# Optimization experiments

Hardware: AMD Instinct MI355X
Metric: run time of the kernel (lower is better)

## Reference

```python
import jax, jax.numpy as jnp
import numpy as np

N = 100_000      # nodes
E = 3_200_000    # edges (avg degree 32)
F_IN = 172       # raw node features
HID = 32         # hid_channels
ENC = 8          # encoding_dim
H, C = 2, 16     # heads, per-head channels (TransformerConv 32 -> 2x16)
OUT = 2          # classes
INV_SQRT_C = 1.0 / np.sqrt(C).astype(np.float32)


def setup_inputs() -> dict:
    key = jax.random.key(0)
    ks = jax.random.split(key, 40)
    p = lambda k, shape: (jax.random.normal(k, shape, dtype=jnp.float32) * 0.05)
    return {
        # data tensors
        "x": jax.random.normal(ks[0], (N, F_IN), dtype=jnp.float32),
        "edge_index": jax.random.randint(ks[1], (2, E), 0, N),
        "node_time": jax.random.uniform(ks[2], (N,), dtype=jnp.float32),
        "edge_time": jax.random.uniform(ks[3], (E, 1), dtype=jnp.float32),
        "node_interval": jax.random.uniform(ks[4], (N, 1), dtype=jnp.float32),
        "node_degree": jax.random.uniform(ks[5], (N, 1), dtype=jnp.float32),
        # TimeEncode(32): cos(Linear(1, 32))
        "Wt": p(ks[6], (1, HID)), "bt": p(ks[7], (HID,)),
        # DegreeEncoder / TemporalFrequencyEncoder: Linear(1, 8)
        "Wd": p(ks[8], (1, ENC)), "bd": p(ks[9], (ENC,)),
        "Wtf": p(ks[10], (1, ENC)), "btf": p(ks[11], (ENC,)),
        # w_enc: Linear(8, 8); w_x: Linear(32, 8)
        "Wenc": p(ks[12], (ENC, ENC)), "benc": p(ks[13], (ENC,)),
        "Wx": p(ks[14], (HID, ENC)), "bx": p(ks[15], (ENC,)),
        # lin: Linear(in_channels, 32)
        "Wlin": p(ks[16], (F_IN, HID)), "blin": p(ks[17], (HID,)),
        # lin_combine: Linear(40, 32)
        "Wcomb": p(ks[18], (HID + ENC, HID)), "bcomb": p(ks[19], (HID,)),
        # TransformerConv projections (32 -> heads*16 = 32)
        "Wq": p(ks[20], (HID, H * C)), "bq": p(ks[21], (H * C,)),
        "Wk": p(ks[22], (HID, H * C)), "bk": p(ks[23], (H * C,)),
        "Wv": p(ks[24], (HID, H * C)), "bv": p(ks[25], (H * C,)),
        "We": p(ks[26], (HID, H * C)), "be": p(ks[27], (H * C,)),
        "Wskip": p(ks[28], (HID, H * C)), "bskip": p(ks[29], (H * C,)),
        # out: Linear(32, out_channels)
        "Wout": p(ks[30], (HID, OUT)), "bout": p(ks[31], (OUT,)),
    }


def _segment_softmax(alpha, seg, num_segments):
    # alpha: [E, H], seg: [E] destination indices
    m = jax.ops.segment_max(alpha, seg, num_segments=num_segments)
    a = jnp.exp(alpha - m[seg])
    s = jax.ops.segment_sum(a, seg, num_segments=num_segments)
    return a / (s[seg] + 1e-16)


def reference(x, edge_index, node_time, edge_time, node_interval, node_degree,
              Wt, bt, Wd, bd, Wtf, btf, Wenc, benc, Wx, bx, Wlin, blin,
              Wcomb, bcomb, Wq, bq, Wk, bk, Wv, bv, We, be, Wskip, bskip,
              Wout, bout):
    src, dst = edge_index[0], edge_index[1]
    n = x.shape[0]

    # ---- time encoding of relative edge time: cos(Linear(rel_t)) ----
    rel_t = node_time[src][:, None] - edge_time               # [E, 1]
    rel_t_enc = jnp.cos(rel_t @ Wt + bt)                      # [E, 32]

    # ---- node encoders + attention-gated combine ----
    h1 = x @ Wlin + blin                                      # [N, 32]
    tf_enc = node_interval @ Wtf + btf                        # [N, 8]
    deg_enc = node_degree @ Wd + bd                           # [N, 8]
    encodings = jnp.stack((tf_enc, deg_enc), axis=1)          # [N, 2, 8]
    enc_proj = jnp.tanh(encodings @ Wenc + benc)              # [N, 2, 8]
    x_proj = jnp.tanh(h1 @ Wx + bx)                           # [N, 8]
    score = jnp.einsum('nke,ne->nk', enc_proj, x_proj)        # [N, 2]
    score = jax.nn.softmax(score, axis=1)
    context = jnp.einsum('nke,nk->ne', encodings, score)      # [N, 8]
    h1 = jnp.concatenate((h1, context), axis=1) @ Wcomb + bcomb  # [N, 32]

    # ---- TransformerConv (heads=2, out=16, concat) with edge features ----
    q = (h1 @ Wq + bq).reshape(n, H, C)
    k = (h1 @ Wk + bk).reshape(n, H, C)
    v = (h1 @ Wv + bv).reshape(n, H, C)
    e = (rel_t_enc @ We + be).reshape(-1, H, C)               # [E, H, C]

    k_e = k[src] + e                                          # [E, H, C]
    alpha = jnp.einsum('ehc,ehc->eh', q[dst], k_e) * INV_SQRT_C
    alpha = _segment_softmax(alpha, dst, n)                   # [E, H]
    msg = (v[src] + e) * alpha[..., None]                     # [E, H, C]
    agg = jax.ops.segment_sum(msg, dst, num_segments=n)       # [N, H, C]
    h2 = agg.reshape(n, H * C) + (h1 @ Wskip + bskip)         # root_weight skip

    out = h2 @ Wout + bout                                    # [N, 2]
    return jax.nn.log_softmax(out, axis=1)
```

## Files before the change

kernel.cpp:

```cpp
#include <hip/hip_runtime.h>
#include <hip/hip_bf16.h>
#include <cstdint>


#define FIN 172
#define INV_SQRT_C 0.25f

typedef _Float16 f16x8 __attribute__((ext_vector_type(8)));
typedef float f32x4 __attribute__((ext_vector_type(4)));

__device__ __forceinline__ uint32_t cvt_pk_bf16(float lo, float hi) {
    uint32_t r;
    asm("v_cvt_pk_bf16_f32 %0, %1, %2" : "=v"(r) : "v"(lo), "v"(hi));
    return r;
}
__device__ __forceinline__ float bflo(uint32_t u) {
    union { uint32_t i; float f; } x; x.i = u << 16; return x.f;
}
__device__ __forceinline__ float bfhi(uint32_t u) {
    union { uint32_t i; float f; } x; x.i = u & 0xFFFF0000u; return x.f;
}
__device__ __forceinline__ void pk_atomic_add_bf16(void* addr, uint32_t data) {
    asm volatile("global_atomic_pk_add_bf16 %0, %1, off"
                 :: "v"((uint64_t)(uintptr_t)addr), "v"(data) : "memory");
}

__global__ __launch_bounds__(256) void k1_lin(
    const float* __restrict__ x, const float* __restrict__ Wlin,
    const float* __restrict__ blin, float* __restrict__ h1pre, int n)
{
    const int lane = threadIdx.x & 63;
    const int g = lane >> 4, m = lane & 15;

    f16x8 Bf[6][2];
    #pragma unroll
    for (int s = 0; s < 6; ++s) {
        #pragma unroll
        for (int i = 0; i < 8; ++i) {
            const int k = s * 32 + g * 8 + i;
            Bf[s][0][i] = (_Float16)((k < FIN) ? Wlin[k * 32 + m] : 0.f);
            Bf[s][1][i] = (_Float16)((k < FIN) ? Wlin[k * 32 + 16 + m] : 0.f);
        }
    }
    const float b0 = blin[m], b1 = blin[16 + m];

    const int wid = blockIdx.x * 4 + (threadIdx.x >> 6);
    const int nW  = gridDim.x * 4;
    const int nChunks = (n + 15) / 16;

    for (int c = wid; c < nChunks; c += nW) {
        const int row = c * 16 + m;
        const bool rv = row < n;
        const float* xr = x + (size_t)row * FIN;

        f32x4 acc0 = {0.f, 0.f, 0.f, 0.f};
        f32x4 acc1 = {0.f, 0.f, 0.f, 0.f};
        #pragma unroll
        for (int s = 0; s < 6; ++s) {
            f16x8 A;
            #pragma unroll
            for (int i = 0; i < 8; ++i) {
                const int k = s * 32 + g * 8 + i;
                A[i] = (_Float16)((rv && k < FIN) ? xr[k] : 0.f);
            }
            acc0 = __builtin_amdgcn_mfma_f32_16x16x32_f16(A, Bf[s][0], acc0, 0, 0, 0);
            acc1 = __builtin_amdgcn_mfma_f32_16x16x32_f16(A, Bf[s][1], acc1, 0, 0, 0);
        }
        #pragma unroll
        for (int r = 0; r < 4; ++r) {
            const int node = c * 16 + 4 * g + r;
            if (node < n) {
                h1pre[(size_t)node * 32 + m]      = acc0[r] + b0;
                h1pre[(size_t)node * 32 + 16 + m] = acc1[r] + b1;
            }
        }
    }
}

template <int K, int O>
__device__ __forceinline__ void matvecKO(const float* __restrict__ v,
                                         const float* __restrict__ W,
                                         const float* __restrict__ B,
                                         float* __restrict__ out)
{
    #pragma unroll
    for (int o4 = 0; o4 < O / 4; ++o4) {
        float a0 = B[o4 * 4 + 0], a1 = B[o4 * 4 + 1];
        float a2 = B[o4 * 4 + 2], a3 = B[o4 * 4 + 3];
        #pragma unroll
        for (int k = 0; k < K; ++k) {
            float4 wv = *reinterpret_cast<const float4*>(&W[k * O + o4 * 4]);
            float hv = v[k];
            a0 = fmaf(hv, wv.x, a0);
            a1 = fmaf(hv, wv.y, a1);
            a2 = fmaf(hv, wv.z, a2);
            a3 = fmaf(hv, wv.w, a3);
        }
        out[o4 * 4 + 0] = a0; out[o4 * 4 + 1] = a1;
        out[o4 * 4 + 2] = a2; out[o4 * 4 + 3] = a3;
    }
}

__global__ __launch_bounds__(256) void k2_enc(
    const float* __restrict__ h1pre,
    const float* __restrict__ node_interval, const float* __restrict__ node_degree,
    const float* __restrict__ Wtf, const float* __restrict__ btf,
    const float* __restrict__ Wd,  const float* __restrict__ bd,
    const float* __restrict__ Wenc, const float* __restrict__ benc,
    const float* __restrict__ Wx,  const float* __restrict__ bx,
    const float* __restrict__ Wcomb, const float* __restrict__ bcomb,
    const float* __restrict__ Wq,  const float* __restrict__ bq,
    const float* __restrict__ Wk,  const float* __restrict__ bk,
    const float* __restrict__ Wv,  const float* __restrict__ bv,
    const float* __restrict__ Wskip, const float* __restrict__ bskip,
    uint32_t* __restrict__ q32, uint32_t* __restrict__ kv32,
    float* __restrict__ skipb, int n)
{
    __shared__ __align__(16) float sWenc[64], sWx[256];
    __shared__ float sWtf[8], sbtf[8], sWd[8], sbd[8], sbenc[8], sbx[8];
    __shared__ __align__(16) _Float16 v40s[256][72];
    __shared__ __align__(16) _Float16 h1s[256][40];

    const int t = threadIdx.x;
    if (t < 8) {
        sWtf[t] = Wtf[t]; sbtf[t] = btf[t];
        sWd[t]  = Wd[t];  sbd[t]  = bd[t];
        sbenc[t] = benc[t]; sbx[t] = bx[t];
    }
    if (t < 64) sWenc[t] = Wenc[t];
    if (t < 256) sWx[t] = Wx[t];

    const int nid = blockIdx.x * 256 + t;
    const bool active = nid < n;

    __syncthreads();

    if (active) {
        float h1p[32];
        const float2* hp = reinterpret_cast<const float2*>(h1pre + (size_t)nid * 32);
        #pragma unroll
        for (int i = 0; i < 16; ++i) {
            float2 v2 = hp[i];
            h1p[2 * i] = v2.x; h1p[2 * i + 1] = v2.y;
        }
        const float ti = node_interval[nid], dg = node_degree[nid];
        float tf[8], de[8];
        #pragma unroll
        for (int j = 0; j < 8; ++j) {
            tf[j] = fmaf(ti, sWtf[j], sbtf[j]);
            de[j] = fmaf(dg, sWd[j], sbd[j]);
        }
        float xp[8];
        matvecKO<32, 8>(h1p, sWx, sbx, xp);
        #pragma unroll
        for (int o = 0; o < 8; ++o) xp[o] = tanhf(xp[o]);

        float ep0[8], ep1[8];
        matvecKO<8, 8>(tf, sWenc, sbenc, ep0);
        matvecKO<8, 8>(de, sWenc, sbenc, ep1);
        float sc0 = 0.f, sc1 = 0.f;
        #pragma unroll
        for (int o = 0; o < 8; ++o) {
            sc0 = fmaf(tanhf(ep0[o]), xp[o], sc0);
            sc1 = fmaf(tanhf(ep1[o]), xp[o], sc1);
        }
        const float mm = fmaxf(sc0, sc1);
        const float e0 = __expf(sc0 - mm), e1 = __expf(sc1 - mm);
        const float inv = 1.f / (e0 + e1);
        const float s0 = e0 * inv, s1 = e1 * inv;

        #pragma unroll
        for (int i = 0; i < 32; ++i) v40s[t][i] = (_Float16)h1p[i];
        #pragma unroll
        for (int j = 0; j < 8; ++j)
            v40s[t][32 + j] = (_Float16)fmaf(s0, tf[j], s1 * de[j]);
    } else {
        #pragma unroll
        for (int i = 0; i < 40; ++i) v40s[t][i] = (_Float16)0.f;
    }
    #pragma unroll
    for (int i = 40; i < 64; ++i) v40s[t][i] = (_Float16)0.f;

    __syncthreads();

    const int lane = t & 63;
    const int g = lane >> 4, m = lane & 15;
    const int wv = t >> 6;
    const int node0 = blockIdx.x * 256;

    f16x8 Bc0[2], Bc1[2];
    #pragma unroll
    for (int s = 0; s < 2; ++s)
        #pragma unroll
        for (int i = 0; i < 8; ++i) {
            const int k = s * 32 + g * 8 + i;
            Bc0[s][i] = (_Float16)((k < 40) ? Wcomb[k * 32 + m] : 0.f);
            Bc1[s][i] = (_Float16)((k < 40) ? Wcomb[k * 32 + 16 + m] : 0.f);
        }
    const float bc0 = bcomb[m], bc1 = bcomb[16 + m];

    for (int c = wv; c < 16; c += 4) {
        f32x4 a0 = {0.f, 0.f, 0.f, 0.f};
        f32x4 a1 = {0.f, 0.f, 0.f, 0.f};
        #pragma unroll
        for (int s = 0; s < 2; ++s) {
            const f16x8 A = *reinterpret_cast<const f16x8*>(&v40s[c * 16 + m][s * 32 + g * 8]);
            a0 = __builtin_amdgcn_mfma_f32_16x16x32_f16(A, Bc0[s], a0, 0, 0, 0);
            a1 = __builtin_amdgcn_mfma_f32_16x16x32_f16(A, Bc1[s], a1, 0, 0, 0);
        }
        #pragma unroll
        for (int r = 0; r < 4; ++r) {
            const int nb = c * 16 + 4 * g + r;
            h1s[nb][m]      = (_Float16)(a0[r] + bc0);
            h1s[nb][16 + m] = (_Float16)(a1[r] + bc1);
        }
    }
    __syncthreads();

    f16x8 Bq0, Bq1, Bk0, Bk1, Bv0, Bv1, Bs0, Bs1;
    #pragma unroll
    for (int i = 0; i < 8; ++i) {
        const int k = g * 8 + i;
        Bq0[i] = (_Float16)Wq[k * 32 + m];     Bq1[i] = (_Float16)Wq[k * 32 + 16 + m];
        Bk0[i] = (_Float16)Wk[k * 32 + m];     Bk1[i] = (_Float16)Wk[k * 32 + 16 + m];
        Bv0[i] = (_Float16)Wv[k * 32 + m];     Bv1[i] = (_Float16)Wv[k * 32 + 16 + m];
        Bs0[i] = (_Float16)Wskip[k * 32 + m];  Bs1[i] = (_Float16)Wskip[k * 32 + 16 + m];
    }
    const float bq0 = bq[m], bq1 = bq[16 + m];
    const float bk0 = bk[m], bk1 = bk[16 + m];
    const float bv0 = bv[m], bv1 = bv[16 + m];
    const float bs0 = bskip[m], bs1 = bskip[16 + m];

    for (int c = wv; c < 16; c += 4) {
        const f16x8 A = *reinterpret_cast<const f16x8*>(&h1s[c * 16 + m][g * 8]);

        f32x4 aq0 = {0.f,0.f,0.f,0.f}, aq1 = {0.f,0.f,0.f,0.f};
        f32x4 ak0 = {0.f,0.f,0.f,0.f}, ak1 = {0.f,0.f,0.f,0.f};
        f32x4 av0 = {0.f,0.f,0.f,0.f}, av1 = {0.f,0.f,0.f,0.f};
        f32x4 as0 = {0.f,0.f,0.f,0.f}, as1 = {0.f,0.f,0.f,0.f};
        aq0 = __builtin_amdgcn_mfma_f32_16x16x32_f16(A, Bq0, aq0, 0, 0, 0);
        aq1 = __builtin_amdgcn_mfma_f32_16x16x32_f16(A, Bq1, aq1, 0, 0, 0);
        ak0 = __builtin_amdgcn_mfma_f32_16x16x32_f16(A, Bk0, ak0, 0, 0, 0);
        ak1 = __builtin_amdgcn_mfma_f32_16x16x32_f16(A, Bk1, ak1, 0, 0, 0);
        av0 = __builtin_amdgcn_mfma_f32_16x16x32_f16(A, Bv0, av0, 0, 0, 0);
        av1 = __builtin_amdgcn_mfma_f32_16x16x32_f16(A, Bv1, av1, 0, 0, 0);
        as0 = __builtin_amdgcn_mfma_f32_16x16x32_f16(A, Bs0, as0, 0, 0, 0);
        as1 = __builtin_amdgcn_mfma_f32_16x16x32_f16(A, Bs1, as1, 0, 0, 0);

        #pragma unroll
        for (int r = 0; r < 4; ++r) {
            const int node = node0 + c * 16 + 4 * g + r;
            if (node < n) {
                q32[(size_t)node * 16 + m] =
                    cvt_pk_bf16(aq0[r] + bq0, aq1[r] + bq1);
                uint2 kvd;
                kvd.x = cvt_pk_bf16(ak0[r] + bk0, ak1[r] + bk1);
                kvd.y = cvt_pk_bf16(av0[r] + bv0, av1[r] + bv1);
                *reinterpret_cast<uint2*>(kv32 + (size_t)node * 32 + 2 * m) = kvd;
                skipb[(size_t)node * 32 + m]      = as0[r] + bs0;
                skipb[(size_t)node * 32 + 16 + m] = as1[r] + bs1;
            }
        }
    }
}

__global__ __launch_bounds__(256) void k3_edge(
    const int* __restrict__ ei, const float* __restrict__ node_time,
    const float* __restrict__ edge_time,
    const uint32_t* __restrict__ qp, const uint32_t* __restrict__ kvp,
    const float* __restrict__ Wt, const float* __restrict__ bt,
    const float* __restrict__ We, const float* __restrict__ be,
    unsigned short* __restrict__ agg, unsigned short* __restrict__ den,
    int numE, int nTiles)
{
    const int lane = threadIdx.x & 63;
    const int g = lane >> 4;
    const int m = lane & 15;

    float wtr[8], btr[8];
    f16x8 B0, B1;
    #pragma unroll
    for (int i = 0; i < 8; ++i) {
        const int k = g * 8 + i;
        wtr[i] = Wt[k];
        btr[i] = bt[k];
        B0[i] = (_Float16)We[k * 32 + m];
        B1[i] = (_Float16)We[k * 32 + 16 + m];
    }
    const float be0 = be[m], be1 = be[16 + m];

    const int wid = blockIdx.x * (blockDim.x >> 6) + (threadIdx.x >> 6);
    const int nW  = gridDim.x * (blockDim.x >> 6);

    int tile = wid;
    if (tile >= nTiles) return;

    int srcm = 0, dstm = 0;
    float et = 0.f;
    {
        const int eA = tile * 16 + m;
        if (eA < numE) {
            srcm = ei[eA];
            dstm = ei[numE + eA];
            et   = edge_time[eA];
        }
    }

    while (true) {
        const float nt = node_time[srcm];
        int srcr[4], dstr[4];
        uint32_t qw[4];
        uint2 kvw[4];
        #pragma unroll
        for (int r = 0; r < 4; ++r) {
            const int j = g * 4 + r;
            srcr[r] = __shfl(srcm, j);
            dstr[r] = __shfl(dstm, j);
            qw[r]  = qp[(size_t)dstr[r] * 16 + m];
            kvw[r] = *reinterpret_cast<const uint2*>(
                         kvp + (size_t)srcr[r] * 32 + 2 * m);
        }

        const int ntile = tile + nW;
        int nsrc = 0, ndst = 0;
        float net = 0.f;
        if (ntile < nTiles) {
            const int eA = ntile * 16 + m;
            if (eA < numE) {
                nsrc = ei[eA];
                ndst = ei[numE + eA];
                net  = edge_time[eA];
            }
        }

        const float rel = nt - et;
        f16x8 A;
        #pragma unroll
        for (int i = 0; i < 8; ++i)
            A[i] = (_Float16)__cosf(fmaf(rel, wtr[i], btr[i]));

        f32x4 acc0 = {0.f, 0.f, 0.f, 0.f};
        f32x4 acc1 = {0.f, 0.f, 0.f, 0.f};
        acc0 = __builtin_amdgcn_mfma_f32_16x16x32_f16(A, B0, acc0, 0, 0, 0);
        acc1 = __builtin_amdgcn_mfma_f32_16x16x32_f16(A, B1, acc1, 0, 0, 0);

        const int e0 = tile * 16;
        #pragma unroll
        for (int r = 0; r < 4; ++r) {
            if (e0 + g * 4 + r < numE) {
                const float ef0 = acc0[r] + be0;
                const float ef1 = acc1[r] + be1;

                const uint32_t uq = qw[r];
                const uint32_t uk = kvw[r].x, uv = kvw[r].y;
                const float q0 = bflo(uq), q1 = bfhi(uq);
                const float k0 = bflo(uk), k1 = bfhi(uk);
                const float v0 = bflo(uv), v1 = bfhi(uv);

                float p0 = q0 * (k0 + ef0);
                float p1 = q1 * (k1 + ef1);
                #pragma unroll
                for (int s = 1; s < 16; s <<= 1) {
                    p0 += __shfl_xor(p0, s);
                    p1 += __shfl_xor(p1, s);
                }
                const float w0 = __expf(p0 * INV_SQRT_C);
                const float w1 = __expf(p1 * INV_SQRT_C);

                const float t0 = w0 * (v0 + ef0);
                const float t1 = w1 * (v1 + ef1);
                const float x0 = __shfl_xor(t0, 1);
                const float x1 = __shfl_xor(t1, 1);
                const uint32_t data = (m & 1) ? cvt_pk_bf16(x1, t1)
                                              : cvt_pk_bf16(t0, x0);
                const int choff = (m & 1) ? (15 + m) : m;
                pk_atomic_add_bf16(agg + (size_t)dstr[r] * 32 + choff, data);

                if (m == 0)
                    pk_atomic_add_bf16(den + (size_t)dstr[r] * 2,
                                       cvt_pk_bf16(w0, w1));
            }
        }

        if (ntile >= nTiles) break;
        tile = ntile; srcm = nsrc; dstm = ndst; et = net;
    }
}

__global__ __launch_bounds__(256) void k4_out(
    const unsigned short* __restrict__ agg, const unsigned short* __restrict__ den,
    const float* __restrict__ skipb,
    const float* __restrict__ Wout, const float* __restrict__ bout,
    float* __restrict__ out, int n)
{
    __shared__ float sW[64];
    __shared__ float sb[2];
    const int t = threadIdx.x;
    if (t < 64) sW[t] = Wout[t];
    if (t < 2) sb[t] = bout[t];
    __syncthreads();

    const int nid = blockIdx.x * 256 + t;
    if (nid >= n) return;

    const uint32_t ud = reinterpret_cast<const uint32_t*>(den)[nid];
    const float inv0 = 1.f / (bflo(ud) + 1e-16f);
    const float inv1 = 1.f / (bfhi(ud) + 1e-16f);
    const uint32_t* ag = reinterpret_cast<const uint32_t*>(agg) + (size_t)nid * 16;
    const float*    sk = skipb + (size_t)nid * 32;

    float o0 = sb[0], o1 = sb[1];
    #pragma unroll
    for (int p = 0; p < 16; ++p) {
        const uint32_t u = ag[p];
        const float iv = (p < 8) ? inv0 : inv1;
        const float hLo = fmaf(bflo(u), iv, sk[2 * p]);
        const float hHi = fmaf(bfhi(u), iv, sk[2 * p + 1]);
        o0 = fmaf(hLo, sW[(2 * p) * 2],     o0);
        o1 = fmaf(hLo, sW[(2 * p) * 2 + 1], o1);
        o0 = fmaf(hHi, sW[(2 * p + 1) * 2],     o0);
        o1 = fmaf(hHi, sW[(2 * p + 1) * 2 + 1], o1);
    }
    const float mm = fmaxf(o0, o1);
    const float lse = mm + __logf(__expf(o0 - mm) + __expf(o1 - mm));
    out[(size_t)nid * 2 + 0] = o0 - lse;
    out[(size_t)nid * 2 + 1] = o1 - lse;
}

extern "C" void kernel_launch(void* const* d_in, const int* in_sizes, int n_in,
                              void* d_out, int out_size, void* d_ws, size_t ws_size,
                              hipStream_t stream)
{
    const float* x             = (const float*)d_in[0];
    const int*   ei            = (const int*)  d_in[1];
    const float* node_time     = (const float*)d_in[2];
    const float* edge_time     = (const float*)d_in[3];
    const float* node_interval = (const float*)d_in[4];
    const float* node_degree   = (const float*)d_in[5];
    const float* Wt    = (const float*)d_in[6];  const float* bt    = (const float*)d_in[7];
    const float* Wd    = (const float*)d_in[8];  const float* bd    = (const float*)d_in[9];
    const float* Wtf   = (const float*)d_in[10]; const float* btf   = (const float*)d_in[11];
    const float* Wenc  = (const float*)d_in[12]; const float* benc  = (const float*)d_in[13];
    const float* Wx    = (const float*)d_in[14]; const float* bx    = (const float*)d_in[15];
    const float* Wlin  = (const float*)d_in[16]; const float* blin  = (const float*)d_in[17];
    const float* Wcomb = (const float*)d_in[18]; const float* bcomb = (const float*)d_in[19];
    const float* Wq    = (const float*)d_in[20]; const float* bq    = (const float*)d_in[21];
    const float* Wk    = (const float*)d_in[22]; const float* bk    = (const float*)d_in[23];
    const float* Wv    = (const float*)d_in[24]; const float* bv    = (const float*)d_in[25];
    const float* We    = (const float*)d_in[26]; const float* be    = (const float*)d_in[27];
    const float* Wskip = (const float*)d_in[28]; const float* bskip = (const float*)d_in[29];
    const float* Wout  = (const float*)d_in[30]; const float* bout  = (const float*)d_in[31];

    const int n    = in_sizes[2];
    const int numE = in_sizes[3];

    char* base = (char*)d_ws;
    uint32_t* q32  = (uint32_t*)base; base += (size_t)n * 16 * 4;
    uint32_t* kv32 = (uint32_t*)base; base += (size_t)n * 32 * 4;
    float* skipb = (float*)base; base += (size_t)n * 32 * 4;
    float* h1pre = (float*)base; base += (size_t)n * 32 * 4;
    unsigned short* agg = (unsigned short*)base; base += (size_t)n * 32 * 2;
    unsigned short* den = (unsigned short*)base; base += (size_t)n * 2 * 2;

    hipMemsetAsync(agg, 0, (size_t)n * (32 * 2 + 2 * 2), stream);

    k1_lin<<<512, 256, 0, stream>>>(x, Wlin, blin, h1pre, n);

    k2_enc<<<(n + 255) / 256, 256, 0, stream>>>(
        h1pre, node_interval, node_degree,
        Wtf, btf, Wd, bd, Wenc, benc, Wx, bx, Wcomb, bcomb,
        Wq, bq, Wk, bk, Wv, bv, Wskip, bskip,
        q32, kv32, skipb, n);

    const int nTiles = (numE + 15) / 16;
    k3_edge<<<4096, 256, 0, stream>>>(
        ei, node_time, edge_time, q32, kv32,
        Wt, bt, We, be, agg, den, numE, nTiles);

    k4_out<<<(n + 255) / 256, 256, 0, stream>>>(
        agg, den, skipb, Wout, bout, (float*)d_out, n);
}
```

Baseline: 423.0 us.

## Project edge messages and skip through Wout before aggregation to shrink atomics

Uses linearity of the final Wout projection: each edge message is reduced per head to two output logits through a 16-lane shuffle reduction. Each edge then issues three small packed-bf16 atomics (head0 logits, head1 logits, softmax denominators) in place of a 32-channel atomic row plus a denominator atomic. The skip path is likewise projected to two floats in k2, which cuts skip buffer traffic. The cost is extra shuffle reductions per edge, and summing projected values in bf16 may change rounding error.

```diff
diff --git a/kernel.cpp b/kernel.cpp
--- a/kernel.cpp
+++ b/kernel.cpp
@@ -113,8 +113,9 @@
     const float* __restrict__ Wk,  const float* __restrict__ bk,
     const float* __restrict__ Wv,  const float* __restrict__ bv,
     const float* __restrict__ Wskip, const float* __restrict__ bskip,
+    const float* __restrict__ Wout,
     uint32_t* __restrict__ q32, uint32_t* __restrict__ kv32,
-    float* __restrict__ skipb, int n)
+    float2* __restrict__ skip2, int n)
 {
     __shared__ __align__(16) float sWenc[64], sWx[256];
     __shared__ float sWtf[8], sbtf[8], sWd[8], sbd[8], sbenc[8], sbx[8];
@@ -230,6 +231,8 @@
     const float bk0 = bk[m], bk1 = bk[16 + m];
     const float bv0 = bv[m], bv1 = bv[16 + m];
     const float bs0 = bskip[m], bs1 = bskip[16 + m];
+    const float wo00 = Wout[m * 2],        wo01 = Wout[m * 2 + 1];
+    const float wo10 = Wout[(16 + m) * 2], wo11 = Wout[(16 + m) * 2 + 1];
 
     for (int c = wv; c < 16; c += 4) {
         const f16x8 A = *reinterpret_cast<const f16x8*>(&h1s[c * 16 + m][g * 8]);
@@ -250,6 +253,14 @@
         #pragma unroll
         for (int r = 0; r < 4; ++r) {
             const int node = node0 + c * 16 + 4 * g + r;
+            const float sv0 = as0[r] + bs0, sv1 = as1[r] + bs1;
+            float u0 = fmaf(sv0, wo00, sv1 * wo10);
+            float u1 = fmaf(sv0, wo01, sv1 * wo11);
+            #pragma unroll
+            for (int s = 1; s < 16; s <<= 1) {
+                u0 += __shfl_xor(u0, s);
+                u1 += __shfl_xor(u1, s);
+            }
             if (node < n) {
                 q32[(size_t)node * 16 + m] =
                     cvt_pk_bf16(aq0[r] + bq0, aq1[r] + bq1);
@@ -257,8 +268,7 @@
                 kvd.x = cvt_pk_bf16(ak0[r] + bk0, ak1[r] + bk1);
                 kvd.y = cvt_pk_bf16(av0[r] + bv0, av1[r] + bv1);
                 *reinterpret_cast<uint2*>(kv32 + (size_t)node * 32 + 2 * m) = kvd;
-                skipb[(size_t)node * 32 + m]      = as0[r] + bs0;
-                skipb[(size_t)node * 32 + 16 + m] = as1[r] + bs1;
+                if (m == 0) skip2[node] = make_float2(u0, u1);
             }
         }
     }
@@ -270,8 +280,8 @@
     const uint32_t* __restrict__ qp, const uint32_t* __restrict__ kvp,
     const float* __restrict__ Wt, const float* __restrict__ bt,
     const float* __restrict__ We, const float* __restrict__ be,
-    unsigned short* __restrict__ agg, unsigned short* __restrict__ den,
-    int numE, int nTiles)
+    const float* __restrict__ Wout,
+    unsigned short* __restrict__ acc, int numE, int nTiles)
 {
     const int lane = threadIdx.x & 63;
     const int g = lane >> 4;
@@ -288,6 +298,8 @@
         B1[i] = (_Float16)We[k * 32 + 16 + m];
     }
     const float be0 = be[m], be1 = be[16 + m];
+    const float wo00 = Wout[m * 2],        wo01 = Wout[m * 2 + 1];
+    const float wo10 = Wout[(16 + m) * 2], wo11 = Wout[(16 + m) * 2 + 1];
 
     const int wid = blockIdx.x * (blockDim.x >> 6) + (threadIdx.x >> 6);
     const int nW  = gridDim.x * (blockDim.x >> 6);
@@ -369,16 +381,18 @@
 
                 const float t0 = w0 * (v0 + ef0);
                 const float t1 = w1 * (v1 + ef1);
-                const float x0 = __shfl_xor(t0, 1);
-                const float x1 = __shfl_xor(t1, 1);
-                const uint32_t data = (m & 1) ? cvt_pk_bf16(x1, t1)
-                                              : cvt_pk_bf16(t0, x0);
-                const int choff = (m & 1) ? (15 + m) : m;
-                pk_atomic_add_bf16(agg + (size_t)dstr[r] * 32 + choff, data);
-
-                if (m == 0)
-                    pk_atomic_add_bf16(den + (size_t)dstr[r] * 2,
-                                       cvt_pk_bf16(w0, w1));
+                float u00 = t0 * wo00, u01 = t0 * wo01;
+                float u10 = t1 * wo10, u11 = t1 * wo11;
+                #pragma unroll
+                for (int s = 1; s < 16; s <<= 1) {
+                    u00 += __shfl_xor(u00, s); u01 += __shfl_xor(u01, s);
+                    u10 += __shfl_xor(u10, s); u11 += __shfl_xor(u11, s);
+                }
+
+                unsigned short* row = acc + (size_t)dstr[r] * 32;
+                if (m == 0) pk_atomic_add_bf16(row,     cvt_pk_bf16(u00, u01));
+                if (m == 1) pk_atomic_add_bf16(row + 2, cvt_pk_bf16(u10, u11));
+                if (m == 2) pk_atomic_add_bf16(row + 4, cvt_pk_bf16(w0,  w1));
             }
         }
 
@@ -388,39 +402,20 @@
 }
 
 __global__ __launch_bounds__(256) void k4_out(
-    const unsigned short* __restrict__ agg, const unsigned short* __restrict__ den,
-    const float* __restrict__ skipb,
-    const float* __restrict__ Wout, const float* __restrict__ bout,
-    float* __restrict__ out, int n)
-{
-    __shared__ float sW[64];
-    __shared__ float sb[2];
-    const int t = threadIdx.x;
-    if (t < 64) sW[t] = Wout[t];
-    if (t < 2) sb[t] = bout[t];
-    __syncthreads();
-
-    const int nid = blockIdx.x * 256 + t;
+    const unsigned short* __restrict__ acc, const float2* __restrict__ skip2,
+    const float* __restrict__ bout, float* __restrict__ out, int n)
+{
+    const int nid = blockIdx.x * 256 + threadIdx.x;
     if (nid >= n) return;
 
-    const uint32_t ud = reinterpret_cast<const uint32_t*>(den)[nid];
-    const float inv0 = 1.f / (bflo(ud) + 1e-16f);
-    const float inv1 = 1.f / (bfhi(ud) + 1e-16f);
-    const uint32_t* ag = reinterpret_cast<const uint32_t*>(agg) + (size_t)nid * 16;
-    const float*    sk = skipb + (size_t)nid * 32;
-
-    float o0 = sb[0], o1 = sb[1];
-    #pragma unroll
-    for (int p = 0; p < 16; ++p) {
-        const uint32_t u = ag[p];
-        const float iv = (p < 8) ? inv0 : inv1;
-        const float hLo = fmaf(bflo(u), iv, sk[2 * p]);
-        const float hHi = fmaf(bfhi(u), iv, sk[2 * p + 1]);
-        o0 = fmaf(hLo, sW[(2 * p) * 2],     o0);
-        o1 = fmaf(hLo, sW[(2 * p) * 2 + 1], o1);
-        o0 = fmaf(hHi, sW[(2 * p + 1) * 2],     o0);
-        o1 = fmaf(hHi, sW[(2 * p + 1) * 2 + 1], o1);
-    }
+    const uint4 u = *reinterpret_cast<const uint4*>(acc + (size_t)nid * 32);
+    const float inv0 = 1.f / (bflo(u.z) + 1e-16f);
+    const float inv1 = 1.f / (bfhi(u.z) + 1e-16f);
+    const float2 sk = skip2[nid];
+
+    const float o0 = bflo(u.x) * inv0 + bflo(u.y) * inv1 + sk.x + bout[0];
+    const float o1 = bfhi(u.x) * inv0 + bfhi(u.y) * inv1 + sk.y + bout[1];
+
     const float mm = fmaxf(o0, o1);
     const float lse = mm + __logf(__expf(o0 - mm) + __expf(o1 - mm));
     out[(size_t)nid * 2 + 0] = o0 - lse;
@@ -457,26 +452,25 @@
     char* base = (char*)d_ws;
     uint32_t* q32  = (uint32_t*)base; base += (size_t)n * 16 * 4;
     uint32_t* kv32 = (uint32_t*)base; base += (size_t)n * 32 * 4;
-    float* skipb = (float*)base; base += (size_t)n * 32 * 4;
     float* h1pre = (float*)base; base += (size_t)n * 32 * 4;
-    unsigned short* agg = (unsigned short*)base; base += (size_t)n * 32 * 2;
-    unsigned short* den = (unsigned short*)base; base += (size_t)n * 2 * 2;
-
-    hipMemsetAsync(agg, 0, (size_t)n * (32 * 2 + 2 * 2), stream);
+    float2* skip2 = (float2*)base; base += (size_t)n * 2 * 4;
+    unsigned short* acc = (unsigned short*)base; base += (size_t)n * 32 * 2;
+
+    hipMemsetAsync(acc, 0, (size_t)n * 32 * 2, stream);
 
     k1_lin<<<512, 256, 0, stream>>>(x, Wlin, blin, h1pre, n);
 
     k2_enc<<<(n + 255) / 256, 256, 0, stream>>>(
         h1pre, node_interval, node_degree,
         Wtf, btf, Wd, bd, Wenc, benc, Wx, bx, Wcomb, bcomb,
-        Wq, bq, Wk, bk, Wv, bv, Wskip, bskip,
-        q32, kv32, skipb, n);
+        Wq, bq, Wk, bk, Wv, bv, Wskip, bskip, Wout,
+        q32, kv32, skip2, n);
 
     const int nTiles = (numE + 15) / 16;
     k3_edge<<<4096, 256, 0, stream>>>(
         ei, node_time, edge_time, q32, kv32,
-        Wt, bt, We, be, agg, den, numE, nTiles);
+        Wt, bt, We, be, Wout, acc, numE, nTiles);
 
     k4_out<<<(n + 255) / 256, 256, 0, stream>>>(
-        agg, den, skipb, Wout, bout, (float*)d_out, n);
-}
+        acc, skip2, bout, (float*)d_out, n);
+}
```

New measurement: 578.4 us, median of 2. +36.7%, slower.

## Software-pipeline edge gathers ahead of atomics and pad denominator rows

Applied to the files above, without the earlier changes.

The edge kernel now prefetches the next tile's q/kv gathers and the tile after's edge indices before issuing the current tile's atomics. This lets gather latency overlap with the atomic scatter. The denominator array is padded to a 64-byte stride per node, which spreads its atomics across cache lines at the cost of a larger memset and sparser reads in the output kernel. The atomic helper also switches to a compiler builtin and drops the memory clobber on the asm fallback, giving the compiler more freedom to reorder.

```diff
diff --git a/kernel.cpp b/kernel.cpp
--- a/kernel.cpp
+++ b/kernel.cpp
@@ -8,6 +8,7 @@
 
 typedef _Float16 f16x8 __attribute__((ext_vector_type(8)));
 typedef float f32x4 __attribute__((ext_vector_type(4)));
+typedef short s16x2 __attribute__((ext_vector_type(2)));
 
 __device__ __forceinline__ uint32_t cvt_pk_bf16(float lo, float hi) {
     uint32_t r;
@@ -20,9 +21,16 @@
 __device__ __forceinline__ float bfhi(uint32_t u) {
     union { uint32_t i; float f; } x; x.i = u & 0xFFFF0000u; return x.f;
 }
+
 __device__ __forceinline__ void pk_atomic_add_bf16(void* addr, uint32_t data) {
+#if __has_builtin(__builtin_amdgcn_global_atomic_fadd_v2bf16)
+    typedef __attribute__((address_space(1))) s16x2* gp1;
+    union { uint32_t u; s16x2 v; } c; c.u = data;
+    __builtin_amdgcn_global_atomic_fadd_v2bf16((gp1)(uintptr_t)addr, c.v);
+#else
     asm volatile("global_atomic_pk_add_bf16 %0, %1, off"
-                 :: "v"((uint64_t)(uintptr_t)addr), "v"(data) : "memory");
+                 :: "v"((uint64_t)(uintptr_t)addr), "v"(data));
+#endif
 }
 
 __global__ __launch_bounds__(256) void k1_lin(
@@ -295,45 +303,31 @@
     int tile = wid;
     if (tile >= nTiles) return;
 
-    int srcm = 0, dstm = 0;
-    float et = 0.f;
+    int srcS = 0, dstS = 0; float etS = 0.f;
     {
         const int eA = tile * 16 + m;
-        if (eA < numE) {
-            srcm = ei[eA];
-            dstm = ei[numE + eA];
-            et   = edge_time[eA];
-        }
+        if (eA < numE) { srcS = ei[eA]; dstS = ei[numE + eA]; etS = edge_time[eA]; }
+    }
+    float ntC = node_time[srcS];
+    float etC = etS;
+    int dstrC[4]; uint32_t qwC[4]; uint2 kvwC[4];
+    #pragma unroll
+    for (int r = 0; r < 4; ++r) {
+        const int j = g * 4 + r;
+        const int s_ = __shfl(srcS, j);
+        dstrC[r] = __shfl(dstS, j);
+        qwC[r]  = qp[(size_t)dstrC[r] * 16 + m];
+        kvwC[r] = *reinterpret_cast<const uint2*>(kvp + (size_t)s_ * 32 + 2 * m);
+    }
+    int ntile = tile + nW;
+    srcS = 0; dstS = 0; etS = 0.f;
+    if (ntile < nTiles) {
+        const int eA = ntile * 16 + m;
+        if (eA < numE) { srcS = ei[eA]; dstS = ei[numE + eA]; etS = edge_time[eA]; }
     }
 
     while (true) {
-        const float nt = node_time[srcm];
-        int srcr[4], dstr[4];
-        uint32_t qw[4];
-        uint2 kvw[4];
-        #pragma unroll
-        for (int r = 0; r < 4; ++r) {
-            const int j = g * 4 + r;
-            srcr[r] = __shfl(srcm, j);
-            dstr[r] = __shfl(dstm, j);
-            qw[r]  = qp[(size_t)dstr[r] * 16 + m];
-            kvw[r] = *reinterpret_cast<const uint2*>(
-                         kvp + (size_t)srcr[r] * 32 + 2 * m);
-        }
-
-        const int ntile = tile + nW;
-        int nsrc = 0, ndst = 0;
-        float net = 0.f;
-        if (ntile < nTiles) {
-            const int eA = ntile * 16 + m;
-            if (eA < numE) {
-                nsrc = ei[eA];
-                ndst = ei[numE + eA];
-                net  = edge_time[eA];
-            }
-        }
-
-        const float rel = nt - et;
+        const float rel = ntC - etC;
         f16x8 A;
         #pragma unroll
         for (int i = 0; i < 8; ++i)
@@ -345,45 +339,68 @@
         acc1 = __builtin_amdgcn_mfma_f32_16x16x32_f16(A, B1, acc1, 0, 0, 0);
 
         const int e0 = tile * 16;
+        uint32_t outD[4], denD[4];
+        int outDst[4];
+        bool outV[4];
         #pragma unroll
         for (int r = 0; r < 4; ++r) {
-            if (e0 + g * 4 + r < numE) {
-                const float ef0 = acc0[r] + be0;
-                const float ef1 = acc1[r] + be1;
-
-                const uint32_t uq = qw[r];
-                const uint32_t uk = kvw[r].x, uv = kvw[r].y;
-                const float q0 = bflo(uq), q1 = bfhi(uq);
-                const float k0 = bflo(uk), k1 = bfhi(uk);
-                const float v0 = bflo(uv), v1 = bfhi(uv);
-
-                float p0 = q0 * (k0 + ef0);
-                float p1 = q1 * (k1 + ef1);
-                #pragma unroll
-                for (int s = 1; s < 16; s <<= 1) {
-                    p0 += __shfl_xor(p0, s);
-                    p1 += __shfl_xor(p1, s);
-                }
-                const float w0 = __expf(p0 * INV_SQRT_C);
-                const float w1 = __expf(p1 * INV_SQRT_C);
-
-                const float t0 = w0 * (v0 + ef0);
-                const float t1 = w1 * (v1 + ef1);
-                const float x0 = __shfl_xor(t0, 1);
-                const float x1 = __shfl_xor(t1, 1);
-                const uint32_t data = (m & 1) ? cvt_pk_bf16(x1, t1)
-                                              : cvt_pk_bf16(t0, x0);
-                const int choff = (m & 1) ? (15 + m) : m;
-                pk_atomic_add_bf16(agg + (size_t)dstr[r] * 32 + choff, data);
-
+            outV[r]   = (e0 + g * 4 + r) < numE;
+            outDst[r] = dstrC[r];
+
+            const float ef0 = acc0[r] + be0;
+            const float ef1 = acc1[r] + be1;
+            const uint32_t uq = qwC[r], uk = kvwC[r].x, uv = kvwC[r].y;
+
+            float p0 = bflo(uq) * (bflo(uk) + ef0);
+            float p1 = bfhi(uq) * (bfhi(uk) + ef1);
+            #pragma unroll
+            for (int s = 1; s < 16; s <<= 1) {
+                p0 += __shfl_xor(p0, s);
+                p1 += __shfl_xor(p1, s);
+            }
+            const float w0 = __expf(p0 * INV_SQRT_C);
+            const float w1 = __expf(p1 * INV_SQRT_C);
+
+            const float t0 = w0 * (bflo(uv) + ef0);
+            const float t1 = w1 * (bfhi(uv) + ef1);
+            const float x0 = __shfl_xor(t0, 1);
+            const float x1 = __shfl_xor(t1, 1);
+            outD[r] = (m & 1) ? cvt_pk_bf16(x1, t1) : cvt_pk_bf16(t0, x0);
+            denD[r] = cvt_pk_bf16(w0, w1);
+        }
+
+        const bool haveN = ntile < nTiles;
+        if (haveN) {
+            ntC = node_time[srcS];
+            etC = etS;
+            #pragma unroll
+            for (int r = 0; r < 4; ++r) {
+                const int j = g * 4 + r;
+                const int s_ = __shfl(srcS, j);
+                dstrC[r] = __shfl(dstS, j);
+                qwC[r]  = qp[(size_t)dstrC[r] * 16 + m];
+                kvwC[r] = *reinterpret_cast<const uint2*>(kvp + (size_t)s_ * 32 + 2 * m);
+            }
+            const int n2 = ntile + nW;
+            srcS = 0; dstS = 0; etS = 0.f;
+            if (n2 < nTiles) {
+                const int eA = n2 * 16 + m;
+                if (eA < numE) { srcS = ei[eA]; dstS = ei[numE + eA]; etS = edge_time[eA]; }
+            }
+        }
+
+        const int choff = (m & 1) ? (15 + m) : m;
+        #pragma unroll
+        for (int r = 0; r < 4; ++r) {
+            if (outV[r]) {
+                pk_atomic_add_bf16(agg + (size_t)outDst[r] * 32 + choff, outD[r]);
                 if (m == 0)
-                    pk_atomic_add_bf16(den + (size_t)dstr[r] * 2,
-                                       cvt_pk_bf16(w0, w1));
-            }
-        }
-
-        if (ntile >= nTiles) break;
-        tile = ntile; srcm = nsrc; dstm = ndst; et = net;
+                    pk_atomic_add_bf16(den + (size_t)outDst[r] * 32, denD[r]);
+            }
+        }
+
+        if (!haveN) break;
+        tile = ntile; ntile += nW;
     }
 }
 
@@ -403,7 +420,7 @@
     const int nid = blockIdx.x * 256 + t;
     if (nid >= n) return;
 
-    const uint32_t ud = reinterpret_cast<const uint32_t*>(den)[nid];
+    const uint32_t ud = reinterpret_cast<const uint32_t*>(den)[(size_t)nid * 16];
     const float inv0 = 1.f / (bflo(ud) + 1e-16f);
     const float inv1 = 1.f / (bfhi(ud) + 1e-16f);
     const uint32_t* ag = reinterpret_cast<const uint32_t*>(agg) + (size_t)nid * 16;
@@ -460,9 +477,9 @@
     float* skipb = (float*)base; base += (size_t)n * 32 * 4;
     float* h1pre = (float*)base; base += (size_t)n * 32 * 4;
     unsigned short* agg = (unsigned short*)base; base += (size_t)n * 32 * 2;
-    unsigned short* den = (unsigned short*)base; base += (size_t)n * 2 * 2;
-
-    hipMemsetAsync(agg, 0, (size_t)n * (32 * 2 + 2 * 2), stream);
+    unsigned short* den = (unsigned short*)base; base += (size_t)n * 32 * 2;
+
+    hipMemsetAsync(agg, 0, (size_t)n * 128, stream);
 
     k1_lin<<<512, 256, 0, stream>>>(x, Wlin, blin, h1pre, n);
 
```

Result: faster. 407.5 us (-3.7%).

## Bucket edges by destination block and aggregate in LDS instead of global atomics

Applied to the files above, without the earlier changes.

Adds a per-call counting sort of edges into 128-node destination buckets (count, scan, scatter kernels) that packs src, local dst and a half-precision relative time into a payload. The edge kernel then runs one block per bucket, loads q into LDS, accumulates messages and denominators with fp32 LDS atomics, and fuses the output projection and log-softmax, removing the separate output kernel. This is meant to replace scattered global bf16 atomics and the agg memset. In exchange it adds three preprocessing kernels, one of them a single-block scan, plus extra edge-array traffic. The per-bucket edge count is uneven, which can leave blocks imbalanced.

```diff
diff --git a/kernel.cpp b/kernel.cpp
--- a/kernel.cpp
+++ b/kernel.cpp
@@ -5,6 +5,7 @@
 
 #define FIN 172
 #define INV_SQRT_C 0.25f
+#define CHUNK 8192
 
 typedef _Float16 f16x8 __attribute__((ext_vector_type(8)));
 typedef float f32x4 __attribute__((ext_vector_type(4)));
@@ -19,10 +20,6 @@
 }
 __device__ __forceinline__ float bfhi(uint32_t u) {
     union { uint32_t i; float f; } x; x.i = u & 0xFFFF0000u; return x.f;
-}
-__device__ __forceinline__ void pk_atomic_add_bf16(void* addr, uint32_t data) {
-    asm volatile("global_atomic_pk_add_bf16 %0, %1, off"
-                 :: "v"((uint64_t)(uintptr_t)addr), "v"(data) : "memory");
 }
 
 __global__ __launch_bounds__(256) void k1_lin(
@@ -264,76 +261,168 @@
     }
 }
 
-__global__ __launch_bounds__(256) void k3_edge(
+__global__ __launch_bounds__(256) void kA_count(
+    const int* __restrict__ ei, int* __restrict__ cnt, int numE, int B)
+{
+    __shared__ int hist[784];
+    const int t = threadIdx.x;
+    for (int i = t; i < B; i += 256) hist[i] = 0;
+    __syncthreads();
+
+    const int stride = gridDim.x * 256;
+    for (int e = blockIdx.x * 256 + t; e < numE; e += stride)
+        atomicAdd(&hist[ei[numE + e] >> 7], 1);
+    __syncthreads();
+
+    for (int i = t; i < B; i += 256)
+        if (hist[i]) atomicAdd(&cnt[i], hist[i]);
+}
+
+__global__ __launch_bounds__(1024) void kB_scan(
+    const int* __restrict__ cnt, int* __restrict__ rowptr,
+    int* __restrict__ cursor, int B)
+{
+    __shared__ int sh[1024];
+    const int t = threadIdx.x;
+    const int v = (t < B) ? cnt[t] : 0;
+    sh[t] = v; __syncthreads();
+    for (int off = 1; off < 1024; off <<= 1) {
+        int add = (t >= off) ? sh[t - off] : 0;
+        __syncthreads();
+        sh[t] += add;
+        __syncthreads();
+    }
+    if (t < B) {
+        const int excl = sh[t] - v;
+        rowptr[t] = excl;
+        cursor[t] = excl;
+        if (t == B - 1) rowptr[B] = sh[t];
+    }
+}
+
+__global__ __launch_bounds__(256) void kC_scatter(
     const int* __restrict__ ei, const float* __restrict__ node_time,
-    const float* __restrict__ edge_time,
+    const float* __restrict__ edge_time, int* __restrict__ cursor,
+    uint2* __restrict__ payload, int numE, int B)
+{
+    __shared__ uint32_t pairs[CHUNK];
+    __shared__ int hist[784];
+    __shared__ int base[784];
+
+    const int t = threadIdx.x;
+    const int e0 = blockIdx.x * CHUNK;
+    const int cntC = min(CHUNK, numE - e0);
+
+    for (int i = t; i < B; i += 256) hist[i] = 0;
+    __syncthreads();
+
+    #pragma unroll
+    for (int i = 0; i < CHUNK / 256; ++i) {
+        const int slot = i * 256 + t;
+        if (slot < cntC) {
+            const int dst = ei[numE + e0 + slot];
+            const int b = dst >> 7;
+            const int p = atomicAdd(&hist[b], 1);
+            pairs[slot] = (uint32_t)p | ((uint32_t)(dst & 127) << 13)
+                                      | ((uint32_t)b << 20);
+        }
+    }
+    __syncthreads();
+
+    for (int j = t; j < B; j += 256)
+        base[j] = hist[j] ? atomicAdd(&cursor[j], hist[j]) : 0;
+    __syncthreads();
+
+    #pragma unroll
+    for (int i = 0; i < CHUNK / 256; ++i) {
+        const int slot = i * 256 + t;
+        if (slot < cntC) {
+            const uint32_t pr = pairs[slot];
+            const int p  = pr & 0x1FFF;
+            const int dl = (pr >> 13) & 127;
+            const int b  = pr >> 20;
+            const int e  = e0 + slot;
+            const int src = ei[e];
+            const float rel = node_time[src] - edge_time[e];
+            union { _Float16 h; unsigned short s; } rb;
+            rb.h = (_Float16)rel;
+            uint2 pl;
+            pl.x = (uint32_t)src;
+            pl.y = (uint32_t)rb.s | ((uint32_t)dl << 16);
+            payload[base[b] + p] = pl;
+        }
+    }
+}
+
+__global__ __launch_bounds__(256) void k3_bucket(
+    const uint2* __restrict__ payload, const int* __restrict__ rowptr,
     const uint32_t* __restrict__ qp, const uint32_t* __restrict__ kvp,
     const float* __restrict__ Wt, const float* __restrict__ bt,
     const float* __restrict__ We, const float* __restrict__ be,
-    unsigned short* __restrict__ agg, unsigned short* __restrict__ den,
-    int numE, int nTiles)
-{
-    const int lane = threadIdx.x & 63;
-    const int g = lane >> 4;
-    const int m = lane & 15;
+    const float* __restrict__ skipb,
+    const float* __restrict__ Wout, const float* __restrict__ bout,
+    float* __restrict__ out, int n)
+{
+    __shared__ uint32_t qlds[128 * 16];
+    __shared__ float agg[128 * 33];
+    __shared__ float den[256];
+    __shared__ float sW[64];
+    __shared__ float sb2[2];
+
+    const int t = threadIdx.x;
+    const int bkt = blockIdx.x;
+    const int node0 = bkt << 7;
+    const int beg = rowptr[bkt], end = rowptr[bkt + 1];
+
+    #pragma unroll
+    for (int i = 0; i < 8; ++i) {
+        const int idx = i * 256 + t;
+        const int node = node0 + (idx >> 4);
+        qlds[idx] = (node < n) ? qp[(size_t)node * 16 + (idx & 15)] : 0u;
+    }
+    for (int i = t; i < 128 * 33; i += 256) agg[i] = 0.f;
+    if (t < 256) den[t] = 0.f;
+    if (t < 64) sW[t] = Wout[t];
+    if (t < 2)  sb2[t] = bout[t];
+
+    const int lane = t & 63;
+    const int g = lane >> 4, m = lane & 15;
+    const int w = t >> 6;
 
     float wtr[8], btr[8];
-    f16x8 B0, B1;
+    f16x8 B0f, B1f;
     #pragma unroll
     for (int i = 0; i < 8; ++i) {
         const int k = g * 8 + i;
-        wtr[i] = Wt[k];
-        btr[i] = bt[k];
-        B0[i] = (_Float16)We[k * 32 + m];
-        B1[i] = (_Float16)We[k * 32 + 16 + m];
+        wtr[i] = Wt[k]; btr[i] = bt[k];
+        B0f[i] = (_Float16)We[k * 32 + m];
+        B1f[i] = (_Float16)We[k * 32 + 16 + m];
     }
     const float be0 = be[m], be1 = be[16 + m];
 
-    const int wid = blockIdx.x * (blockDim.x >> 6) + (threadIdx.x >> 6);
-    const int nW  = gridDim.x * (blockDim.x >> 6);
-
-    int tile = wid;
-    if (tile >= nTiles) return;
-
-    int srcm = 0, dstm = 0;
-    float et = 0.f;
-    {
-        const int eA = tile * 16 + m;
-        if (eA < numE) {
-            srcm = ei[eA];
-            dstm = ei[numE + eA];
-            et   = edge_time[eA];
-        }
-    }
-
-    while (true) {
-        const float nt = node_time[srcm];
-        int srcr[4], dstr[4];
-        uint32_t qw[4];
-        uint2 kvw[4];
+    __syncthreads();
+
+    const int nEdges = end - beg;
+    for (int t16 = w * 16; t16 < nEdges; t16 += 64) {
+        const int eA = beg + t16 + m;
+        uint2 pl = make_uint2(0u, 0u);
+        if (eA < end) pl = payload[eA];
+        const int srcm = (int)pl.x;
+        const int dlm  = (pl.y >> 16) & 127;
+        union { unsigned short s; _Float16 h; } rb;
+        rb.s = (unsigned short)(pl.y & 0xFFFF);
+        const float rel = (float)rb.h;
+
+        int dlr[4]; uint2 kvw[4]; uint32_t qw[4];
         #pragma unroll
         for (int r = 0; r < 4; ++r) {
             const int j = g * 4 + r;
-            srcr[r] = __shfl(srcm, j);
-            dstr[r] = __shfl(dstm, j);
-            qw[r]  = qp[(size_t)dstr[r] * 16 + m];
-            kvw[r] = *reinterpret_cast<const uint2*>(
-                         kvp + (size_t)srcr[r] * 32 + 2 * m);
-        }
-
-        const int ntile = tile + nW;
-        int nsrc = 0, ndst = 0;
-        float net = 0.f;
-        if (ntile < nTiles) {
-            const int eA = ntile * 16 + m;
-            if (eA < numE) {
-                nsrc = ei[eA];
-                ndst = ei[numE + eA];
-                net  = edge_time[eA];
-            }
-        }
-
-        const float rel = nt - et;
+            const int s_ = __shfl(srcm, j);
+            dlr[r] = __shfl(dlm, j);
+            kvw[r] = *reinterpret_cast<const uint2*>(kvp + (size_t)s_ * 32 + 2 * m);
+            qw[r]  = qlds[dlr[r] * 16 + m];
+        }
+
         f16x8 A;
         #pragma unroll
         for (int i = 0; i < 8; ++i)
@@ -341,24 +430,18 @@
 
         f32x4 acc0 = {0.f, 0.f, 0.f, 0.f};
         f32x4 acc1 = {0.f, 0.f, 0.f, 0.f};
-        acc0 = __builtin_amdgcn_mfma_f32_16x16x32_f16(A, B0, acc0, 0, 0, 0);
-        acc1 = __builtin_amdgcn_mfma_f32_16x16x32_f16(A, B1, acc1, 0, 0, 0);
-
-        const int e0 = tile * 16;
+        acc0 = __builtin_amdgcn_mfma_f32_16x16x32_f16(A, B0f, acc0, 0, 0, 0);
+        acc1 = __builtin_amdgcn_mfma_f32_16x16x32_f16(A, B1f, acc1, 0, 0, 0);
+
         #pragma unroll
         for (int r = 0; r < 4; ++r) {
-            if (e0 + g * 4 + r < numE) {
+            if (t16 + g * 4 + r < nEdges) {
                 const float ef0 = acc0[r] + be0;
                 const float ef1 = acc1[r] + be1;
-
-                const uint32_t uq = qw[r];
-                const uint32_t uk = kvw[r].x, uv = kvw[r].y;
-                const float q0 = bflo(uq), q1 = bfhi(uq);
-                const float k0 = bflo(uk), k1 = bfhi(uk);
-                const float v0 = bflo(uv), v1 = bfhi(uv);
-
-                float p0 = q0 * (k0 + ef0);
-                float p1 = q1 * (k1 + ef1);
+                const uint32_t uq = qw[r], uk = kvw[r].x, uv = kvw[r].y;
+
+                float p0 = bflo(uq) * (bflo(uk) + ef0);
+                float p1 = bfhi(uq) * (bfhi(uk) + ef1);
                 #pragma unroll
                 for (int s = 1; s < 16; s <<= 1) {
                     p0 += __shfl_xor(p0, s);
@@ -367,64 +450,40 @@
                 const float w0 = __expf(p0 * INV_SQRT_C);
                 const float w1 = __expf(p1 * INV_SQRT_C);
 
-                const float t0 = w0 * (v0 + ef0);
-                const float t1 = w1 * (v1 + ef1);
-                const float x0 = __shfl_xor(t0, 1);
-                const float x1 = __shfl_xor(t1, 1);
-                const uint32_t data = (m & 1) ? cvt_pk_bf16(x1, t1)
-                                              : cvt_pk_bf16(t0, x0);
-                const int choff = (m & 1) ? (15 + m) : m;
-                pk_atomic_add_bf16(agg + (size_t)dstr[r] * 32 + choff, data);
-
-                if (m == 0)
-                    pk_atomic_add_bf16(den + (size_t)dstr[r] * 2,
-                                       cvt_pk_bf16(w0, w1));
+                const float t0 = w0 * (bflo(uv) + ef0);
+                const float t1 = w1 * (bfhi(uv) + ef1);
+
+                atomicAdd(&agg[dlr[r] * 33 + m],      t0);
+                atomicAdd(&agg[dlr[r] * 33 + 16 + m], t1);
+                if (m == 0) {
+                    atomicAdd(&den[dlr[r] * 2],     w0);
+                    atomicAdd(&den[dlr[r] * 2 + 1], w1);
+                }
             }
         }
-
-        if (ntile >= nTiles) break;
-        tile = ntile; srcm = nsrc; dstm = ndst; et = net;
-    }
-}
-
-__global__ __launch_bounds__(256) void k4_out(
-    const unsigned short* __restrict__ agg, const unsigned short* __restrict__ den,
-    const float* __restrict__ skipb,
-    const float* __restrict__ Wout, const float* __restrict__ bout,
-    float* __restrict__ out, int n)
-{
-    __shared__ float sW[64];
-    __shared__ float sb[2];
-    const int t = threadIdx.x;
-    if (t < 64) sW[t] = Wout[t];
-    if (t < 2) sb[t] = bout[t];
-    __syncthreads();
-
-    const int nid = blockIdx.x * 256 + t;
-    if (nid >= n) return;
-
-    const uint32_t ud = reinterpret_cast<const uint32_t*>(den)[nid];
-    const float inv0 = 1.f / (bflo(ud) + 1e-16f);
-    const float inv1 = 1.f / (bfhi(ud) + 1e-16f);
-    const uint32_t* ag = reinterpret_cast<const uint32_t*>(agg) + (size_t)nid * 16;
-    const float*    sk = skipb + (size_t)nid * 32;
-
-    float o0 = sb[0], o1 = sb[1];
-    #pragma unroll
-    for (int p = 0; p < 16; ++p) {
-        const uint32_t u = ag[p];
-        const float iv = (p < 8) ? inv0 : inv1;
-        const float hLo = fmaf(bflo(u), iv, sk[2 * p]);
-        const float hHi = fmaf(bfhi(u), iv, sk[2 * p + 1]);
-        o0 = fmaf(hLo, sW[(2 * p) * 2],     o0);
-        o1 = fmaf(hLo, sW[(2 * p) * 2 + 1], o1);
-        o0 = fmaf(hHi, sW[(2 * p + 1) * 2],     o0);
-        o1 = fmaf(hHi, sW[(2 * p + 1) * 2 + 1], o1);
-    }
-    const float mm = fmaxf(o0, o1);
-    const float lse = mm + __logf(__expf(o0 - mm) + __expf(o1 - mm));
-    out[(size_t)nid * 2 + 0] = o0 - lse;
-    out[(size_t)nid * 2 + 1] = o1 - lse;
+    }
+    __syncthreads();
+
+    if (t < 128) {
+        const int node = node0 + t;
+        if (node < n) {
+            const float inv0 = 1.f / (den[t * 2]     + 1e-16f);
+            const float inv1 = 1.f / (den[t * 2 + 1] + 1e-16f);
+            const float* sk = skipb + (size_t)node * 32;
+            float o0 = sb2[0], o1 = sb2[1];
+            #pragma unroll
+            for (int c = 0; c < 32; ++c) {
+                const float iv = (c < 16) ? inv0 : inv1;
+                const float h = fmaf(agg[t * 33 + c], iv, sk[c]);
+                o0 = fmaf(h, sW[c * 2],     o0);
+                o1 = fmaf(h, sW[c * 2 + 1], o1);
+            }
+            const float mm = fmaxf(o0, o1);
+            const float lse = mm + __logf(__expf(o0 - mm) + __expf(o1 - mm));
+            out[(size_t)node * 2 + 0] = o0 - lse;
+            out[(size_t)node * 2 + 1] = o1 - lse;
+        }
+    }
 }
 
 extern "C" void kernel_launch(void* const* d_in, const int* in_sizes, int n_in,
@@ -453,16 +512,26 @@
 
     const int n    = in_sizes[2];
     const int numE = in_sizes[3];
+    const int B    = (n + 127) >> 7;
 
     char* base = (char*)d_ws;
     uint32_t* q32  = (uint32_t*)base; base += (size_t)n * 16 * 4;
     uint32_t* kv32 = (uint32_t*)base; base += (size_t)n * 32 * 4;
     float* skipb = (float*)base; base += (size_t)n * 32 * 4;
     float* h1pre = (float*)base; base += (size_t)n * 32 * 4;
-    unsigned short* agg = (unsigned short*)base; base += (size_t)n * 32 * 2;
-    unsigned short* den = (unsigned short*)base; base += (size_t)n * 2 * 2;
-
-    hipMemsetAsync(agg, 0, (size_t)n * (32 * 2 + 2 * 2), stream);
+    uint2* payload = (uint2*)base; base += (size_t)numE * 8;
+    int* rowptr = (int*)base; base += (size_t)(B + 1) * 4;
+    int* cnt    = (int*)base; base += (size_t)B * 4;
+    int* cursor = (int*)base; base += (size_t)B * 4;
+
+    hipMemsetAsync(cnt, 0, (size_t)B * 4, stream);
+
+    kA_count<<<1024, 256, 0, stream>>>(ei, cnt, numE, B);
+    kB_scan<<<1, 1024, 0, stream>>>(cnt, rowptr, cursor, B);
+
+    const int nChunks = (numE + CHUNK - 1) / CHUNK;
+    kC_scatter<<<nChunks, 256, 0, stream>>>(
+        ei, node_time, edge_time, cursor, payload, numE, B);
 
     k1_lin<<<512, 256, 0, stream>>>(x, Wlin, blin, h1pre, n);
 
@@ -472,11 +541,7 @@
         Wq, bq, Wk, bk, Wv, bv, Wskip, bskip,
         q32, kv32, skipb, n);
 
-    const int nTiles = (numE + 15) / 16;
-    k3_edge<<<4096, 256, 0, stream>>>(
-        ei, node_time, edge_time, q32, kv32,
-        Wt, bt, We, be, agg, den, numE, nTiles);
-
-    k4_out<<<(n + 255) / 256, 256, 0, stream>>>(
-        agg, den, skipb, Wout, bout, (float*)d_out, n);
-}
+    k3_bucket<<<B, 256, 0, stream>>>(
+        payload, rowptr, q32, kv32, Wt, bt, We, be,
+        skipb, Wout, bout, (float*)d_out, n);
+}
```

Result: slower. 1.003 ms (+137.2%).
